# Kernel optimization log

Measured on AMD Instinct MI355X. Metric: run time of the kernel, lower is better.

Reference implementation:

```python
import jax, jax.numpy as jnp
import numpy as np

N, IN_DIM, OUT_DIM = 50000, 256, 64
K, DELTA_D = 8, 8            # k = out_dim // (ndim // init_k) = 64 // (64 // 8)
M = 1638400                  # edges
ROUTIT, TAU = 4, 1.0
EPS = 1e-12                  # F.normalize eps


def _l2norm(v, n, k, dd):
    # F.normalize over last dim of (n, k, dd) view, flattened back to (n, k*dd)
    v = v.reshape(n, k, dd)
    nrm = jnp.sqrt(jnp.sum(v * v, axis=2, keepdims=True))
    v = v / jnp.maximum(nrm, EPS)
    return v.reshape(n, k * dd)


def setup_inputs() -> dict:
    key = jax.random.key(0)
    k1, k2, k3, k4 = jax.random.split(key, 4)
    x = jax.random.normal(k1, (N, IN_DIM), dtype=jnp.float32)
    src_trg = jax.random.randint(k2, (2, M), 0, N, dtype=jnp.int64)
    std = 1.0 / np.sqrt(OUT_DIM)
    weight = jax.random.uniform(k3, (IN_DIM, OUT_DIM), dtype=jnp.float32, minval=-std, maxval=std)
    bias = jax.random.uniform(k4, (OUT_DIM,), dtype=jnp.float32, minval=-std, maxval=std)
    return {"x": x, "src_trg": src_trg, "weight": weight, "bias": bias}


def reference(x, src_trg, weight, bias):
    trg, src = src_trg[0], src_trg[1]
    n = x.shape[0]
    d = K * DELTA_D
    # DimReduceLayer + leaky_relu + per-capsule L2 normalize
    h = jax.nn.leaky_relu(x @ weight + bias)          # (n, d)
    h = _l2norm(h, n, K, DELTA_D)
    # RoutingLayer normalizes again (idempotent up to eps, kept for fidelity)
    h = _l2norm(h, n, K, DELTA_D)
    z = h[src].reshape(M, K, DELTA_D)                  # gather source capsules
    c = h
    for _ in range(ROUTIT):
        ct = c[trg].reshape(M, K, DELTA_D)             # gather target capsules
        p = jnp.sum(z * ct, axis=2)                    # (m, k) per-edge capsule scores
        p = jax.nn.softmax(p / TAU, axis=1)
        ws = (p[:, :, None] * z).reshape(M, d)         # weighted messages
        c = c.at[trg].add(ws)                          # scatter-add into targets
        c = _l2norm(c, n, K, DELTA_D)
    return c
```

## Files before the change

kernel.cpp:

```cpp
#include <hip/hip_runtime.h>
#include <math.h>

#define IN_DIM 256
#define OUT_D 64
#define ROUTIT 4
#define LCAP 48
#define NG 6
#define GBLK 512
#define BSH 7
#define NBMAX 512

__device__ __forceinline__ float dpp_add_xor1(float x) {
    return x + __int_as_float(__builtin_amdgcn_mov_dpp(__float_as_int(x), 0xB1, 0xF, 0xF, true));
}
__device__ __forceinline__ float dpp_add_xor2(float x) {
    return x + __int_as_float(__builtin_amdgcn_mov_dpp(__float_as_int(x), 0x4E, 0xF, 0xF, true));
}
__device__ __forceinline__ float dpp_add_xor8(float x) {
    return x + __int_as_float(__builtin_amdgcn_mov_dpp(__float_as_int(x), 0x128, 0xF, 0xF, true));
}
__device__ __forceinline__ float swz_add_xor4(float x) {
    return x + __int_as_float(__builtin_amdgcn_ds_swizzle(__float_as_int(x), 0x101F));
}
__device__ __forceinline__ float swz_add_xor16(float x) {
    return x + __int_as_float(__builtin_amdgcn_ds_swizzle(__float_as_int(x), 0x401F));
}

__device__ __forceinline__ void load8v(float z[8], const float* p) {
    float4 a = *(const float4*)p;
    float4 b = *(const float4*)(p + 4);
    z[0]=a.x; z[1]=a.y; z[2]=a.z; z[3]=a.w;
    z[4]=b.x; z[5]=b.y; z[6]=b.z; z[7]=b.w;
}

__global__ __launch_bounds__(GBLK) void gemm_norm_kernel(
    const float* __restrict__ x, const float* __restrict__ w,
    const float* __restrict__ bias, float* __restrict__ h, int n)
{
    __shared__ float wlds[IN_DIM * OUT_D];
    {
        const float4* wsrc = (const float4*)w;
        float4* wdst = (float4*)wlds;
        #pragma unroll
        for (int i = 0; i < (IN_DIM * OUT_D / 4); i += GBLK)
            wdst[i + threadIdx.x] = wsrc[i + threadIdx.x];
    }
    __syncthreads();

    int lane = threadIdx.x & 63;
    int wv   = threadIdx.x >> 6;
    int c0   = wv * 8;
    int row  = blockIdx.x * 64 + lane;
    int rc   = row < n ? row : n - 1;
    const float* xr = x + (size_t)rc * IN_DIM;

    float acc[8];
    #pragma unroll
    for (int c = 0; c < 8; ++c) acc[c] = bias[c0 + c];

    float4 xa = *(const float4*)(xr);
    float4 xb = *(const float4*)(xr + 4);
    #pragma unroll 2
    for (int k0 = 0; k0 < IN_DIM; k0 += 8) {
        int kn = (k0 + 8 < IN_DIM) ? k0 + 8 : 0;
        float4 na = *(const float4*)(xr + kn);
        float4 nb = *(const float4*)(xr + kn + 4);
        float xs[8] = {xa.x, xa.y, xa.z, xa.w, xb.x, xb.y, xb.z, xb.w};
        const float* wk = wlds + k0 * OUT_D + c0;
        #pragma unroll
        for (int kk = 0; kk < 8; ++kk) {
            float4 w0 = *(const float4*)(wk + kk * OUT_D);
            float4 w1 = *(const float4*)(wk + kk * OUT_D + 4);
            acc[0] = fmaf(xs[kk], w0.x, acc[0]);
            acc[1] = fmaf(xs[kk], w0.y, acc[1]);
            acc[2] = fmaf(xs[kk], w0.z, acc[2]);
            acc[3] = fmaf(xs[kk], w0.w, acc[3]);
            acc[4] = fmaf(xs[kk], w1.x, acc[4]);
            acc[5] = fmaf(xs[kk], w1.y, acc[5]);
            acc[6] = fmaf(xs[kk], w1.z, acc[6]);
            acc[7] = fmaf(xs[kk], w1.w, acc[7]);
        }
        xa = na; xb = nb;
    }

    if (row < n) {
        #pragma unroll
        for (int c = 0; c < 8; ++c) {
            float v = acc[c];
            acc[c] = v > 0.0f ? v : 0.01f * v;
        }
        #pragma unroll
        for (int r = 0; r < 2; ++r) {
            float ss = 0.0f;
            #pragma unroll
            for (int d = 0; d < 8; ++d) ss = fmaf(acc[d], acc[d], ss);
            float inv = 1.0f / fmaxf(sqrtf(ss), 1e-12f);
            #pragma unroll
            for (int d = 0; d < 8; ++d) acc[d] *= inv;
        }
        float* hr = h + (size_t)row * OUT_D + c0;
        float4 o1, o2;
        o1.x=acc[0]; o1.y=acc[1]; o1.z=acc[2]; o1.w=acc[3];
        o2.x=acc[4]; o2.y=acc[5]; o2.z=acc[6]; o2.w=acc[7];
        *(float4*)hr = o1;
        *(float4*)(hr + 4) = o2;
    }
}


__global__ __launch_bounds__(256) void bucket_hist_kernel(
    const int* __restrict__ trg, int m4, int* __restrict__ bucket_counts, int nb)
{
    __shared__ int hist[NBMAX];
    for (int i = threadIdx.x; i < nb; i += 256) hist[i] = 0;
    __syncthreads();
    int i = blockIdx.x * 256 + threadIdx.x;
    if (i < m4) {
        int4 t = ((const int4*)trg)[i];
        atomicAdd(&hist[t.x >> BSH], 1);
        atomicAdd(&hist[t.y >> BSH], 1);
        atomicAdd(&hist[t.z >> BSH], 1);
        atomicAdd(&hist[t.w >> BSH], 1);
    }
    __syncthreads();
    for (int i2 = threadIdx.x; i2 < nb; i2 += 256) {
        int c = hist[i2];
        if (c) atomicAdd(&bucket_counts[i2], c);
    }
}

__global__ __launch_bounds__(64) void bucket_scan_kernel(
    const int* __restrict__ bucket_counts, int* __restrict__ bucket_base,
    int* __restrict__ bucket_cursor, int nb, int n, int m, int* __restrict__ row_start)
{
    int lane = threadIdx.x;
    int carry = 0;
    for (int base = 0; base <= nb; base += 64) {
        int i = base + lane;
        int v = (i < nb) ? bucket_counts[i] : 0;
        int s = v;
        #pragma unroll
        for (int off = 1; off < 64; off <<= 1) {
            int t = __shfl_up(s, off, 64);
            if (lane >= off) s += t;
        }
        if (i <= nb) {
            int exc = carry + s - v;
            bucket_base[i]   = exc;
            bucket_cursor[i] = exc;
        }
        carry += __shfl(s, 63, 64);
    }
    if (lane == 0) row_start[n] = m;
}

__global__ __launch_bounds__(256) void partition_kernel(
    const int* __restrict__ trg, const int* __restrict__ src, int m4,
    int2* __restrict__ epairs, int* __restrict__ bucket_cursor, int nb)
{
    __shared__ int hist[NBMAX];
    __shared__ int runbase[NBMAX];
    for (int i = threadIdx.x; i < nb; i += 256) hist[i] = 0;
    __syncthreads();

    int4 tv[4], sv[4];
    int base4 = blockIdx.x * 1024;
    #pragma unroll
    for (int k = 0; k < 4; ++k) {
        int i4 = base4 + k * 256 + threadIdx.x;
        if (i4 < m4) {
            tv[k] = ((const int4*)trg)[i4];
            sv[k] = ((const int4*)src)[i4];
            atomicAdd(&hist[tv[k].x >> BSH], 1);
            atomicAdd(&hist[tv[k].y >> BSH], 1);
            atomicAdd(&hist[tv[k].z >> BSH], 1);
            atomicAdd(&hist[tv[k].w >> BSH], 1);
        } else {
            tv[k] = make_int4(-1,-1,-1,-1);
            sv[k] = make_int4(0,0,0,0);
        }
    }
    __syncthreads();
    for (int i = threadIdx.x; i < nb; i += 256) {
        int c = hist[i];
        runbase[i] = c ? atomicAdd(&bucket_cursor[i], c) : 0;
    }
    __syncthreads();
    for (int i = threadIdx.x; i < nb; i += 256) hist[i] = 0;
    __syncthreads();
    #pragma unroll
    for (int k = 0; k < 4; ++k) {
        int tt[4] = {tv[k].x, tv[k].y, tv[k].z, tv[k].w};
        int ss[4] = {sv[k].x, sv[k].y, sv[k].z, sv[k].w};
        #pragma unroll
        for (int j = 0; j < 4; ++j) {
            int t = tt[j];
            if (t >= 0) {
                int b = t >> BSH;
                int r = atomicAdd(&hist[b], 1);
                epairs[runbase[b] + r] = make_int2(ss[j], t);
            }
        }
    }
}

__global__ __launch_bounds__(256) void local_csr_kernel(
    const int2* __restrict__ epairs, const int* __restrict__ bucket_base,
    int* __restrict__ row_start, int* __restrict__ edge_src, int n)
{
    __shared__ int hist[128];
    __shared__ int excl[129];
    __shared__ int cursor[128];
    int b = blockIdx.x;
    int ebeg = bucket_base[b], eend = bucket_base[b + 1];
    int node0 = b << BSH;
    if (threadIdx.x < 128) hist[threadIdx.x] = 0;
    __syncthreads();
    for (int e = ebeg + (int)threadIdx.x; e < eend; e += 256) {
        int2 p = epairs[e];
        atomicAdd(&hist[p.y - node0], 1);
    }
    __syncthreads();
    if (threadIdx.x < 64) {
        int lane = threadIdx.x;
        int carry = 0;
        #pragma unroll
        for (int c = 0; c < 2; ++c) {
            int i = c * 64 + lane;
            int v = hist[i];
            int s = v;
            #pragma unroll
            for (int off = 1; off < 64; off <<= 1) {
                int t = __shfl_up(s, off, 64);
                if (lane >= off) s += t;
            }
            excl[i] = carry + s - v;
            carry += __shfl(s, 63, 64);
        }
        if (lane == 0) excl[128] = carry;
    }
    __syncthreads();
    int nh = n - node0; if (nh > 128) nh = 128;
    for (int i = threadIdx.x; i <= nh; i += 256)
        row_start[node0 + i] = ebeg + excl[i];
    if (threadIdx.x < 128) cursor[threadIdx.x] = excl[threadIdx.x];
    __syncthreads();
    for (int e = ebeg + (int)threadIdx.x; e < eend; e += 256) {
        int2 p = epairs[e];
        int r = atomicAdd(&cursor[p.y - node0], 1);
        edge_src[ebeg + r] = p.x;
    }
}

__device__ __forceinline__ void route_group(const float z[8], const float c[8], float acc[8]) {
    float p = z[0] * c[0];
    #pragma unroll
    for (int d = 1; d < 8; ++d) p = fmaf(z[d], c[d], p);
    float ex = __expf(p);
    float sm = dpp_add_xor1(ex);
    sm = dpp_add_xor2(sm);
    sm = dpp_add_xor8(sm);
    float wgt = __fdividef(ex, sm);
    #pragma unroll
    for (int d = 0; d < 8; ++d) acc[d] = fmaf(wgt, z[d], acc[d]);
}

__global__ __launch_bounds__(256, 4) void route_kernel(
    const float* __restrict__ h, const int* __restrict__ row_start,
    const int* __restrict__ edge_src, float* __restrict__ out, int n)
{
    int lane = threadIdx.x & 63;
    int wid  = threadIdx.x >> 6;
    int v = blockIdx.x * 4 + wid;
    if (v >= n) return;
    int beg = row_start[v];
    int deg = row_start[v + 1] - beg;
    int nl  = deg < LCAP ? deg : LCAP;
    int ngroups = (nl + 7) >> 3;

    int k  = (lane & 3) | ((lane >> 1) & 4);
    int eo = ((lane >> 2) & 1) | ((lane >> 3) & 6);

    float c[8];
    load8v(c, h + (size_t)v * OUT_D + k * 8);

    float z[NG][8];
    #pragma unroll
    for (int g = 0; g < NG; ++g) {
        int e = g * 8 + eo;
        if (e < nl) {
            int s = edge_src[beg + e];
            load8v(z[g], h + (size_t)s * OUT_D + k * 8);
        } else {
            #pragma unroll
            for (int d = 0; d < 8; ++d) z[g][d] = 0.0f;
        }
    }

    #pragma unroll
    for (int it = 0; it < ROUTIT; ++it) {
        float acc[8] = {0,0,0,0,0,0,0,0};
        #pragma unroll
        for (int g = 0; g < NG; ++g)
            if (g < ngroups) route_group(z[g], c, acc);
        if (deg > LCAP) {
            for (int e0 = LCAP; e0 < deg; e0 += 8) {
                int e = e0 + eo;
                float zt[8] = {0,0,0,0,0,0,0,0};
                if (e < deg) {
                    int s = edge_src[beg + e];
                    load8v(zt, h + (size_t)s * OUT_D + k * 8);
                }
                route_group(zt, c, acc);
            }
        }
        float ss = 0.0f;
        #pragma unroll
        for (int d = 0; d < 8; ++d) {
            float a = acc[d];
            a = swz_add_xor4(a);
            a = swz_add_xor16(a);
            a += __shfl_xor(a, 32, 64);
            float cv = c[d] + a;
            c[d] = cv;
            ss = fmaf(cv, cv, ss);
        }
        float inv = 1.0f / fmaxf(sqrtf(ss), 1e-12f);
        #pragma unroll
        for (int d = 0; d < 8; ++d) c[d] *= inv;
    }
    if (eo == 0) {
        float* op = out + (size_t)v * OUT_D + k * 8;
        float4 o1, o2;
        o1.x=c[0]; o1.y=c[1]; o1.z=c[2]; o1.w=c[3];
        o2.x=c[4]; o2.y=c[5]; o2.z=c[6]; o2.w=c[7];
        *(float4*)op = o1;
        *(float4*)(op + 4) = o2;
    }
}

extern "C" void kernel_launch(void* const* d_in, const int* in_sizes, int n_in,
                              void* d_out, int out_size, void* d_ws, size_t ws_size,
                              hipStream_t stream)
{
    const float* x       = (const float*)d_in[0];
    const int*   src_trg = (const int*)d_in[1];
    const float* w       = (const float*)d_in[2];
    const float* bias    = (const float*)d_in[3];
    float*       out     = (float*)d_out;

    int n = in_sizes[0] / IN_DIM;
    int m = in_sizes[1] / 2;
    int m4 = m >> 2;
    int nb = (n + 127) >> BSH;
    const int* trg = src_trg;
    const int* src = src_trg + m;

    char* wsb = (char*)d_ws;
    size_t off = 0;
    float* h        = (float*)(wsb + off); off += (size_t)n * OUT_D * sizeof(float);
    int*   rowstart = (int*)(wsb + off);   off += (size_t)(n + 1) * sizeof(int);
    off = (off + 255) & ~(size_t)255;
    int*   edgesrc  = (int*)(wsb + off);   off += (size_t)m * sizeof(int);
    off = (off + 255) & ~(size_t)255;
    int2*  epairs   = (int2*)(wsb + off);  off += (size_t)m * sizeof(int2);
    int*   bcounts  = (int*)(wsb + off);   off += (size_t)(nb + 1) * sizeof(int);
    int*   bbase    = (int*)(wsb + off);   off += (size_t)(nb + 1) * sizeof(int);
    int*   bcursor  = (int*)(wsb + off);   off += (size_t)(nb + 1) * sizeof(int);

    hipMemsetAsync(bcounts, 0, (size_t)(nb + 1) * sizeof(int), stream);
    gemm_norm_kernel<<<(n + 63) / 64, GBLK, 0, stream>>>(x, w, bias, h, n);
    bucket_hist_kernel<<<(m4 + 255) / 256, 256, 0, stream>>>(trg, m4, bcounts, nb);
    bucket_scan_kernel<<<1, 64, 0, stream>>>(bcounts, bbase, bcursor, nb, n, m, rowstart);
    partition_kernel<<<(m4 + 1023) / 1024, 256, 0, stream>>>(trg, src, m4, epairs, bcursor, nb);
    local_csr_kernel<<<nb, 256, 0, stream>>>(epairs, bbase, rowstart, edgesrc, n);
    route_kernel<<<(n + 3) / 4, 256, 0, stream>>>(h, rowstart, edgesrc, out, n);
}
```

Baseline: 301.3 us.

## Register-tile GEMM rows, pack edge pairs into 32 bits, use exp2 routing

The GEMM kernel now computes four rows per thread, reusing each LDS weight load across rows, with a 512x2 launch bound and a quarter as many blocks. The partition kernel processes twice as many edges per block and re-reads trg/src instead of holding them in registers. Each edge becomes one 32-bit word (local target in the high 16 bits, source in the low 16), halving the intermediate traffic in partition and the local CSR build. Routing prescales the capsule by log2(e) and uses exp2f. The packing only holds for node counts below 65536.

```diff
diff --git a/kernel.cpp b/kernel.cpp
--- a/kernel.cpp
+++ b/kernel.cpp
@@ -1,14 +1,15 @@
 #include <hip/hip_runtime.h>
 #include <math.h>
+#include <stdint.h>
 
 #define IN_DIM 256
 #define OUT_D 64
 #define ROUTIT 4
 #define LCAP 48
 #define NG 6
-#define GBLK 512
 #define BSH 7
 #define NBMAX 512
+#define LOG2E 1.4426950408889634f
 
 __device__ __forceinline__ float dpp_add_xor1(float x) {
     return x + __int_as_float(__builtin_amdgcn_mov_dpp(__float_as_int(x), 0xB1, 0xF, 0xF, true));
@@ -33,7 +34,7 @@
     z[4]=b.x; z[5]=b.y; z[6]=b.z; z[7]=b.w;
 }
 
-__global__ __launch_bounds__(GBLK) void gemm_norm_kernel(
+__global__ __launch_bounds__(512, 2) void gemm_norm_kernel(
     const float* __restrict__ x, const float* __restrict__ w,
     const float* __restrict__ bias, float* __restrict__ h, int n)
 {
@@ -42,7 +43,7 @@
         const float4* wsrc = (const float4*)w;
         float4* wdst = (float4*)wlds;
         #pragma unroll
-        for (int i = 0; i < (IN_DIM * OUT_D / 4); i += GBLK)
+        for (int i = 0; i < (IN_DIM * OUT_D / 4); i += 512)
             wdst[i + threadIdx.x] = wsrc[i + threadIdx.x];
     }
     __syncthreads();
@@ -50,60 +51,87 @@
     int lane = threadIdx.x & 63;
     int wv   = threadIdx.x >> 6;
     int c0   = wv * 8;
-    int row  = blockIdx.x * 64 + lane;
-    int rc   = row < n ? row : n - 1;
-    const float* xr = x + (size_t)rc * IN_DIM;
-
-    float acc[8];
-    #pragma unroll
-    for (int c = 0; c < 8; ++c) acc[c] = bias[c0 + c];
-
-    float4 xa = *(const float4*)(xr);
-    float4 xb = *(const float4*)(xr + 4);
-    #pragma unroll 2
+    int base = blockIdx.x * 256;
+
+    const float* xr[4];
+    int rows[4];
+    #pragma unroll
+    for (int r = 0; r < 4; ++r) {
+        rows[r] = base + r * 64 + lane;
+        int rc = rows[r] < n ? rows[r] : n - 1;
+        xr[r] = x + (size_t)rc * IN_DIM;
+    }
+
+    float acc[4][8];
+    #pragma unroll
+    for (int r = 0; r < 4; ++r)
+        #pragma unroll
+        for (int c = 0; c < 8; ++c) acc[r][c] = bias[c0 + c];
+
+    float4 xa[4], xb[4];
+    #pragma unroll
+    for (int r = 0; r < 4; ++r) {
+        xa[r] = *(const float4*)(xr[r]);
+        xb[r] = *(const float4*)(xr[r] + 4);
+    }
+
     for (int k0 = 0; k0 < IN_DIM; k0 += 8) {
         int kn = (k0 + 8 < IN_DIM) ? k0 + 8 : 0;
-        float4 na = *(const float4*)(xr + kn);
-        float4 nb = *(const float4*)(xr + kn + 4);
-        float xs[8] = {xa.x, xa.y, xa.z, xa.w, xb.x, xb.y, xb.z, xb.w};
+        float4 na[4], nb[4];
+        #pragma unroll
+        for (int r = 0; r < 4; ++r) {
+            na[r] = *(const float4*)(xr[r] + kn);
+            nb[r] = *(const float4*)(xr[r] + kn + 4);
+        }
         const float* wk = wlds + k0 * OUT_D + c0;
         #pragma unroll
         for (int kk = 0; kk < 8; ++kk) {
             float4 w0 = *(const float4*)(wk + kk * OUT_D);
             float4 w1 = *(const float4*)(wk + kk * OUT_D + 4);
-            acc[0] = fmaf(xs[kk], w0.x, acc[0]);
-            acc[1] = fmaf(xs[kk], w0.y, acc[1]);
-            acc[2] = fmaf(xs[kk], w0.z, acc[2]);
-            acc[3] = fmaf(xs[kk], w0.w, acc[3]);
-            acc[4] = fmaf(xs[kk], w1.x, acc[4]);
-            acc[5] = fmaf(xs[kk], w1.y, acc[5]);
-            acc[6] = fmaf(xs[kk], w1.z, acc[6]);
-            acc[7] = fmaf(xs[kk], w1.w, acc[7]);
-        }
-        xa = na; xb = nb;
-    }
-
-    if (row < n) {
-        #pragma unroll
-        for (int c = 0; c < 8; ++c) {
-            float v = acc[c];
-            acc[c] = v > 0.0f ? v : 0.01f * v;
-        }
-        #pragma unroll
-        for (int r = 0; r < 2; ++r) {
-            float ss = 0.0f;
-            #pragma unroll
-            for (int d = 0; d < 8; ++d) ss = fmaf(acc[d], acc[d], ss);
-            float inv = 1.0f / fmaxf(sqrtf(ss), 1e-12f);
-            #pragma unroll
-            for (int d = 0; d < 8; ++d) acc[d] *= inv;
-        }
-        float* hr = h + (size_t)row * OUT_D + c0;
-        float4 o1, o2;
-        o1.x=acc[0]; o1.y=acc[1]; o1.z=acc[2]; o1.w=acc[3];
-        o2.x=acc[4]; o2.y=acc[5]; o2.z=acc[6]; o2.w=acc[7];
-        *(float4*)hr = o1;
-        *(float4*)(hr + 4) = o2;
+            #pragma unroll
+            for (int r = 0; r < 4; ++r) {
+                float xs = (kk < 4)
+                    ? ((kk == 0) ? xa[r].x : (kk == 1) ? xa[r].y : (kk == 2) ? xa[r].z : xa[r].w)
+                    : ((kk == 4) ? xb[r].x : (kk == 5) ? xb[r].y : (kk == 6) ? xb[r].z : xb[r].w);
+                acc[r][0] = fmaf(xs, w0.x, acc[r][0]);
+                acc[r][1] = fmaf(xs, w0.y, acc[r][1]);
+                acc[r][2] = fmaf(xs, w0.z, acc[r][2]);
+                acc[r][3] = fmaf(xs, w0.w, acc[r][3]);
+                acc[r][4] = fmaf(xs, w1.x, acc[r][4]);
+                acc[r][5] = fmaf(xs, w1.y, acc[r][5]);
+                acc[r][6] = fmaf(xs, w1.z, acc[r][6]);
+                acc[r][7] = fmaf(xs, w1.w, acc[r][7]);
+            }
+        }
+        #pragma unroll
+        for (int r = 0; r < 4; ++r) { xa[r] = na[r]; xb[r] = nb[r]; }
+    }
+
+    #pragma unroll
+    for (int r = 0; r < 4; ++r) {
+        if (rows[r] < n) {
+            float a[8];
+            #pragma unroll
+            for (int c = 0; c < 8; ++c) {
+                float v = acc[r][c];
+                a[c] = v > 0.0f ? v : 0.01f * v;
+            }
+            #pragma unroll
+            for (int rep = 0; rep < 2; ++rep) {
+                float ss = 0.0f;
+                #pragma unroll
+                for (int d = 0; d < 8; ++d) ss = fmaf(a[d], a[d], ss);
+                float inv = 1.0f / fmaxf(sqrtf(ss), 1e-12f);
+                #pragma unroll
+                for (int d = 0; d < 8; ++d) a[d] *= inv;
+            }
+            float* hr = h + (size_t)rows[r] * OUT_D + c0;
+            float4 o1, o2;
+            o1.x=a[0]; o1.y=a[1]; o1.z=a[2]; o1.w=a[3];
+            o2.x=a[4]; o2.y=a[5]; o2.z=a[6]; o2.w=a[7];
+            *(float4*)hr = o1;
+            *(float4*)(hr + 4) = o2;
+        }
     }
 }
 
@@ -156,28 +184,22 @@
 
 __global__ __launch_bounds__(256) void partition_kernel(
     const int* __restrict__ trg, const int* __restrict__ src, int m4,
-    int2* __restrict__ epairs, int* __restrict__ bucket_cursor, int nb)
+    uint32_t* __restrict__ epack, int* __restrict__ bucket_cursor, int nb)
 {
     __shared__ int hist[NBMAX];
     __shared__ int runbase[NBMAX];
     for (int i = threadIdx.x; i < nb; i += 256) hist[i] = 0;
     __syncthreads();
-
-    int4 tv[4], sv[4];
-    int base4 = blockIdx.x * 1024;
-    #pragma unroll
-    for (int k = 0; k < 4; ++k) {
-        int i4 = base4 + k * 256 + threadIdx.x;
+    int base4 = blockIdx.x * 2048;
+    #pragma unroll
+    for (int j = 0; j < 8; ++j) {
+        int i4 = base4 + j * 256 + threadIdx.x;
         if (i4 < m4) {
-            tv[k] = ((const int4*)trg)[i4];
-            sv[k] = ((const int4*)src)[i4];
-            atomicAdd(&hist[tv[k].x >> BSH], 1);
-            atomicAdd(&hist[tv[k].y >> BSH], 1);
-            atomicAdd(&hist[tv[k].z >> BSH], 1);
-            atomicAdd(&hist[tv[k].w >> BSH], 1);
-        } else {
-            tv[k] = make_int4(-1,-1,-1,-1);
-            sv[k] = make_int4(0,0,0,0);
+            int4 t = ((const int4*)trg)[i4];
+            atomicAdd(&hist[t.x >> BSH], 1);
+            atomicAdd(&hist[t.y >> BSH], 1);
+            atomicAdd(&hist[t.z >> BSH], 1);
+            atomicAdd(&hist[t.w >> BSH], 1);
         }
     }
     __syncthreads();
@@ -189,23 +211,26 @@
     for (int i = threadIdx.x; i < nb; i += 256) hist[i] = 0;
     __syncthreads();
     #pragma unroll
-    for (int k = 0; k < 4; ++k) {
-        int tt[4] = {tv[k].x, tv[k].y, tv[k].z, tv[k].w};
-        int ss[4] = {sv[k].x, sv[k].y, sv[k].z, sv[k].w};
-        #pragma unroll
-        for (int j = 0; j < 4; ++j) {
-            int t = tt[j];
-            if (t >= 0) {
-                int b = t >> BSH;
+    for (int j = 0; j < 8; ++j) {
+        int i4 = base4 + j * 256 + threadIdx.x;
+        if (i4 < m4) {
+            int4 t = ((const int4*)trg)[i4];
+            int4 s = ((const int4*)src)[i4];
+            int tt[4] = {t.x, t.y, t.z, t.w};
+            int ss[4] = {s.x, s.y, s.z, s.w};
+            #pragma unroll
+            for (int q = 0; q < 4; ++q) {
+                int b = tt[q] >> BSH;
                 int r = atomicAdd(&hist[b], 1);
-                epairs[runbase[b] + r] = make_int2(ss[j], t);
+                epack[runbase[b] + r] =
+                    ((uint32_t)(tt[q] & ((1 << BSH) - 1)) << 16) | (uint32_t)ss[q];
             }
         }
     }
 }
 
 __global__ __launch_bounds__(256) void local_csr_kernel(
-    const int2* __restrict__ epairs, const int* __restrict__ bucket_base,
+    const uint32_t* __restrict__ epack, const int* __restrict__ bucket_base,
     int* __restrict__ row_start, int* __restrict__ edge_src, int n)
 {
     __shared__ int hist[128];
@@ -216,10 +241,8 @@
     int node0 = b << BSH;
     if (threadIdx.x < 128) hist[threadIdx.x] = 0;
     __syncthreads();
-    for (int e = ebeg + (int)threadIdx.x; e < eend; e += 256) {
-        int2 p = epairs[e];
-        atomicAdd(&hist[p.y - node0], 1);
-    }
+    for (int e = ebeg + (int)threadIdx.x; e < eend; e += 256)
+        atomicAdd(&hist[epack[e] >> 16], 1);
     __syncthreads();
     if (threadIdx.x < 64) {
         int lane = threadIdx.x;
@@ -246,17 +269,17 @@
     if (threadIdx.x < 128) cursor[threadIdx.x] = excl[threadIdx.x];
     __syncthreads();
     for (int e = ebeg + (int)threadIdx.x; e < eend; e += 256) {
-        int2 p = epairs[e];
-        int r = atomicAdd(&cursor[p.y - node0], 1);
-        edge_src[ebeg + r] = p.x;
-    }
-}
-
-__device__ __forceinline__ void route_group(const float z[8], const float c[8], float acc[8]) {
-    float p = z[0] * c[0];
-    #pragma unroll
-    for (int d = 1; d < 8; ++d) p = fmaf(z[d], c[d], p);
-    float ex = __expf(p);
+        uint32_t p = epack[e];
+        int r = atomicAdd(&cursor[p >> 16], 1);
+        edge_src[ebeg + r] = (int)(p & 0xFFFFu);
+    }
+}
+
+__device__ __forceinline__ void route_group(const float z[8], const float csc[8], float acc[8]) {
+    float p = z[0] * csc[0];
+    #pragma unroll
+    for (int d = 1; d < 8; ++d) p = fmaf(z[d], csc[d], p);
+    float ex = exp2f(p);
     float sm = dpp_add_xor1(ex);
     sm = dpp_add_xor2(sm);
     sm = dpp_add_xor8(sm);
@@ -299,10 +322,13 @@
 
     #pragma unroll
     for (int it = 0; it < ROUTIT; ++it) {
+        float csc[8];
+        #pragma unroll
+        for (int d = 0; d < 8; ++d) csc[d] = c[d] * LOG2E;
         float acc[8] = {0,0,0,0,0,0,0,0};
         #pragma unroll
         for (int g = 0; g < NG; ++g)
-            if (g < ngroups) route_group(z[g], c, acc);
+            if (g < ngroups) route_group(z[g], csc, acc);
         if (deg > LCAP) {
             for (int e0 = LCAP; e0 < deg; e0 += 8) {
                 int e = e0 + eo;
@@ -311,7 +337,7 @@
                     int s = edge_src[beg + e];
                     load8v(zt, h + (size_t)s * OUT_D + k * 8);
                 }
-                route_group(zt, c, acc);
+                route_group(zt, csc, acc);
             }
         }
         float ss = 0.0f;
@@ -358,21 +384,21 @@
 
     char* wsb = (char*)d_ws;
     size_t off = 0;
-    float* h        = (float*)(wsb + off); off += (size_t)n * OUT_D * sizeof(float);
-    int*   rowstart = (int*)(wsb + off);   off += (size_t)(n + 1) * sizeof(int);
+    float*    h        = (float*)(wsb + off);    off += (size_t)n * OUT_D * sizeof(float);
+    int*      rowstart = (int*)(wsb + off);      off += (size_t)(n + 1) * sizeof(int);
     off = (off + 255) & ~(size_t)255;
-    int*   edgesrc  = (int*)(wsb + off);   off += (size_t)m * sizeof(int);
+    int*      edgesrc  = (int*)(wsb + off);      off += (size_t)m * sizeof(int);
     off = (off + 255) & ~(size_t)255;
-    int2*  epairs   = (int2*)(wsb + off);  off += (size_t)m * sizeof(int2);
-    int*   bcounts  = (int*)(wsb + off);   off += (size_t)(nb + 1) * sizeof(int);
-    int*   bbase    = (int*)(wsb + off);   off += (size_t)(nb + 1) * sizeof(int);
-    int*   bcursor  = (int*)(wsb + off);   off += (size_t)(nb + 1) * sizeof(int);
+    uint32_t* epack    = (uint32_t*)(wsb + off); off += (size_t)m * sizeof(uint32_t);
+    int*      bcounts  = (int*)(wsb + off);      off += (size_t)(nb + 1) * sizeof(int);
+    int*      bbase    = (int*)(wsb + off);      off += (size_t)(nb + 1) * sizeof(int);
+    int*      bcursor  = (int*)(wsb + off);      off += (size_t)(nb + 1) * sizeof(int);
 
     hipMemsetAsync(bcounts, 0, (size_t)(nb + 1) * sizeof(int), stream);
-    gemm_norm_kernel<<<(n + 63) / 64, GBLK, 0, stream>>>(x, w, bias, h, n);
+    gemm_norm_kernel<<<(n + 255) / 256, 512, 0, stream>>>(x, w, bias, h, n);
     bucket_hist_kernel<<<(m4 + 255) / 256, 256, 0, stream>>>(trg, m4, bcounts, nb);
     bucket_scan_kernel<<<1, 64, 0, stream>>>(bcounts, bbase, bcursor, nb, n, m, rowstart);
-    partition_kernel<<<(m4 + 1023) / 1024, 256, 0, stream>>>(trg, src, m4, epairs, bcursor, nb);
-    local_csr_kernel<<<nb, 256, 0, stream>>>(epairs, bbase, rowstart, edgesrc, n);
+    partition_kernel<<<(m4 + 2047) / 2048, 256, 0, stream>>>(trg, src, m4, epack, bcursor, nb);
+    local_csr_kernel<<<nb, 256, 0, stream>>>(epack, bbase, rowstart, edgesrc, n);
     route_kernel<<<(n + 3) / 4, 256, 0, stream>>>(h, rowstart, edgesrc, out, n);
 }
```

Result: slower. 318.5 us (+5.7%).
